# Performance work log

Hardware: AMD Instinct MI355X
Metric: run time of the kernel (lower is better)

## Reference

```python
import jax, jax.numpy as jnp
import numpy as np


def quat_to_rot(q):
    # q: [B, 4] = (x, y, z, w); same math as from_quaternion in the source.
    x, y, z, w = q[:, 0], q[:, 1], q[:, 2], q[:, 3]
    tx, ty, tz = 2.0 * x, 2.0 * y, 2.0 * z
    twx, twy, twz = tx * w, ty * w, tz * w
    txx, txy, txz = tx * x, ty * x, tz * x
    tyy, tyz, tzz = ty * y, tz * y, tz * z
    r = jnp.stack([1.0 - (tyy + tzz), txy - twz, txz + twy,
                   txy + twz, 1.0 - (txx + tzz), tyz - twx,
                   txz - twy, tyz + twx, 1.0 - (txx + tyy)], axis=-1)
    return r.reshape(-1, 3, 3)


def matrix_from_params(transfos):
    B, N = transfos.shape
    R = quat_to_rot(transfos[:, :4])
    if N == 10:
        S = jax.vmap(jnp.diag)(transfos[:, -3:])
    else:
        S = jnp.broadcast_to(jnp.eye(3, dtype=transfos.dtype), (B, 3, 3))
    SR = jnp.matmul(S, R)
    if N == 7:
        t = transfos[:, 4:7][..., None]
    else:
        t = jnp.zeros((B, 3, 1), transfos.dtype)
    return jnp.concatenate([SR, t], axis=2)  # [B, 3, 4]


def spatial_transformer_3d(img, transfos, min_ref_grid, max_ref_grid):
    B, H, W, D, C = img.shape  # ref_size_xyz = (W, H, D) per the source
    theta = matrix_from_params(transfos)  # [B, 3, 4]

    xs = jnp.linspace(min_ref_grid[0], max_ref_grid[0], W)
    ys = jnp.linspace(min_ref_grid[1], max_ref_grid[1], H)
    zs = jnp.linspace(min_ref_grid[2], max_ref_grid[2], D)
    mz, my, mx = jnp.meshgrid(zs, ys, xs, indexing='ij')  # (D, H, W), x fastest
    Nel = D * H * W
    grid = jnp.stack([mx.ravel(), my.ravel(), mz.ravel(),
                      jnp.ones(Nel, dtype=img.dtype)], axis=0)  # (4, Nel)
    pts = jnp.einsum('bij,jn->bin', theta, grid)  # (B, 3, Nel)

    Wf, Hf, Df = float(W), float(H), float(D)
    cx = (Wf - 1.0) / (max_ref_grid[0] - min_ref_grid[0])
    cy = (Hf - 1.0) / (max_ref_grid[1] - min_ref_grid[1])
    cz = (Df - 1.0) / (max_ref_grid[2] - min_ref_grid[2])
    ix = cx * pts[:, 0, :] - cx * min_ref_grid[0]
    iy = cy * pts[:, 1, :] - cy * min_ref_grid[1]
    iz = cz * pts[:, 2, :] - cz * min_ref_grid[2]

    # padding_mode in {'zeros','min'}: validity mask for out-of-grid points
    valid = ((ix >= 0.0) & (ix <= Wf - 1.0) &
             (iy >= 0.0) & (iy <= Hf - 1.0) &
             (iz >= 0.0) & (iz <= Df - 1.0)).astype(img.dtype)[..., None]  # (B, Nel, 1)

    ix0 = jnp.clip(jnp.floor(ix), 0.0, Wf - 1.0)
    iy0 = jnp.clip(jnp.floor(iy), 0.0, Hf - 1.0)
    iz0 = jnp.clip(jnp.floor(iz), 0.0, Df - 1.0)

    imf = img.reshape(B, H * W * D, C)
    acc = jnp.zeros((B, Nel, C), img.dtype)
    for ox in (0.0, 1.0):
        for oy in (0.0, 1.0):
            for oz in (0.0, 1.0):
                gx, gy, gz = ix0 + ox, iy0 + oy, iz0 + oz  # corner coords
                w = (jnp.clip(1.0 - jnp.abs(ix - gx), 0.0, 1.0) *
                     jnp.clip(1.0 - jnp.abs(iy - gy), 0.0, 1.0) *
                     jnp.clip(1.0 - jnp.abs(iz - gz), 0.0, 1.0))
                gxi = jnp.clip(gx, 0.0, Wf - 1.0).astype(jnp.int32)
                gyi = jnp.clip(gy, 0.0, Hf - 1.0).astype(jnp.int32)
                gzi = jnp.clip(gz, 0.0, Df - 1.0).astype(jnp.int32)
                lin = (gyi * W + gxi) * D + gzi  # row-major index into [H, W, D]
                v = jnp.take_along_axis(imf, lin[..., None], axis=1)  # (B, Nel, C)
                acc = acc + w[..., None] * v

    # padding_mode == 'min': fill out-of-grid voxels with the per-volume minimum
    fill = jnp.min(img, axis=(1, 2, 3, 4))[:, None, None]  # (B, 1, 1)
    out = valid * acc + (1.0 - valid) * fill
    # grid was flattened in (z, y, x) order with x fastest -> back to (H, W, D)
    out = out.reshape(B, D, H, W, C).transpose(0, 2, 3, 1, 4)
    return out


def setup_inputs() -> dict:
    key = jax.random.key(0)
    k1, k2 = jax.random.split(key)
    img = jax.random.normal(k1, (4, 160, 160, 160, 1), dtype=jnp.float32)
    transfos = jax.random.normal(k2, (4, 7), dtype=jnp.float32)
    return {"img": img, "transfos": transfos}


def reference(img, transfos):
    min_ref_grid = (-1.0, -1.0, -1.0)
    max_ref_grid = (1.0, 1.0, 1.0)
    return spatial_transformer_3d(img, transfos, min_ref_grid, max_ref_grid)
```

## Files before the change

### kernel.cpp

```cpp
#include <hip/hip_runtime.h>

#define HH 160
#define WW 160
#define DD 160
#define BB 4
#define NPB (HH * WW * DD / 4)
#define K1B 256
#define NTZ 10
#define NTX 20
#define NTY 20

typedef float vfloat4 __attribute__((ext_vector_type(4)));

__global__ __launch_bounds__(256) void min_cst_kernel(const float4* __restrict__ img4,
                                                      const float* __restrict__ transfos,
                                                      float* __restrict__ partial,
                                                      double* __restrict__ cst) {
    const int b = blockIdx.y;
    const size_t base = (size_t)b * NPB;
    const int t0 = blockIdx.x * 256 + threadIdx.x;
    const int S = K1B * 256;

    float m = 3.4e38f;
    #pragma unroll
    for (int r = 0; r < 4; r++) {
        const int i0 = t0 + 4 * r * S;
        float4 v0 = img4[base + i0];
        float4 v1 = img4[base + i0 + S];
        float4 v2 = img4[base + i0 + 2 * S];
        float4 v3 = make_float4(3.4e38f, 3.4e38f, 3.4e38f, 3.4e38f);
        if (i0 + 3 * S < NPB) v3 = img4[base + i0 + 3 * S];
        m = fminf(m, fminf(fminf(v0.x, v0.y), fminf(v0.z, v0.w)));
        m = fminf(m, fminf(fminf(v1.x, v1.y), fminf(v1.z, v1.w)));
        m = fminf(m, fminf(fminf(v2.x, v2.y), fminf(v2.z, v2.w)));
        m = fminf(m, fminf(fminf(v3.x, v3.y), fminf(v3.z, v3.w)));
    }

    #pragma unroll
    for (int o = 32; o >= 1; o >>= 1) m = fminf(m, __shfl_down(m, o));
    __shared__ float s[4];
    if ((threadIdx.x & 63) == 0) s[threadIdx.x >> 6] = m;
    __syncthreads();
    if (threadIdx.x == 0)
        partial[b * K1B + blockIdx.x] = fminf(fminf(s[0], s[1]), fminf(s[2], s[3]));

    if (blockIdx.x == 0 && blockIdx.y == 0 && threadIdx.x < BB) {
        const int bb = threadIdx.x;
        const float* q = transfos + bb * 7;
        double x = q[0], y = q[1], z = q[2], w = q[3];
        double tx = 2.0 * x, ty = 2.0 * y, tz = 2.0 * z;
        double twx = tx * w, twy = ty * w, twz = tz * w;
        double txx = tx * x, txy = ty * x, txz = tz * x;
        double tyy = ty * y, tyz = tz * y, tzz = tz * z;
        double R[3][3] = {
            {1.0 - (tyy + tzz), txy - twz,         txz + twy},
            {txy + twz,         1.0 - (txx + tzz), tyz - twx},
            {txz - twy,         tyz + twx,         1.0 - (txx + tyy)}
        };
        double t[3] = {(double)q[4], (double)q[5], (double)q[6]};
        for (int r = 0; r < 3; r++) {
            cst[bb * 12 + r * 4 + 0] = R[r][0];
            cst[bb * 12 + r * 4 + 1] = R[r][1];
            cst[bb * 12 + r * 4 + 2] = R[r][2];
            cst[bb * 12 + r * 4 + 3] = 79.5 * (t[r] - R[r][0] - R[r][1] - R[r][2] + 1.0);
        }
    }
}

__global__ __launch_bounds__(256) void fin_min_kernel(const float* __restrict__ partial,
                                                      float* __restrict__ fill) {
    const int wid = threadIdx.x >> 6, lane = threadIdx.x & 63;
    const float* p = partial + wid * K1B;
    float m = fminf(fminf(p[lane], p[lane + 64]), fminf(p[lane + 128], p[lane + 192]));
    #pragma unroll
    for (int o = 32; o >= 1; o >>= 1) m = fminf(m, __shfl_down(m, o));
    if (lane == 0) fill[wid] = m;
}

__device__ __forceinline__ bool tile_may_be_valid(const double* c, int xt, int yt, int zt) {
    const double X0 = (double)(xt * 8), X1 = X0 + 7.0;
    const double Y0 = (double)(yt * 8), Y1 = Y0 + 7.0;
    const double Z0 = (double)(zt * 16), Z1 = Z0 + 15.0;
    double lo, hi, t;

    lo = c[3]; hi = c[3];
    t = c[0]; if (t >= 0.0) { lo += t * X0; hi += t * X1; } else { lo += t * X1; hi += t * X0; }
    t = c[1]; if (t >= 0.0) { lo += t * Y0; hi += t * Y1; } else { lo += t * Y1; hi += t * Y0; }
    t = c[2]; if (t >= 0.0) { lo += t * Z0; hi += t * Z1; } else { lo += t * Z1; hi += t * Z0; }
    if (hi < -1e-3 || lo > 159.001) return false;

    lo = c[7]; hi = c[7];
    t = c[4]; if (t >= 0.0) { lo += t * X0; hi += t * X1; } else { lo += t * X1; hi += t * X0; }
    t = c[5]; if (t >= 0.0) { lo += t * Y0; hi += t * Y1; } else { lo += t * Y1; hi += t * Y0; }
    t = c[6]; if (t >= 0.0) { lo += t * Z0; hi += t * Z1; } else { lo += t * Z1; hi += t * Z0; }
    if (hi < -1e-3 || lo > 159.001) return false;

    lo = c[11]; hi = c[11];
    t = c[8]; if (t >= 0.0) { lo += t * X0; hi += t * X1; } else { lo += t * X1; hi += t * X0; }
    t = c[9]; if (t >= 0.0) { lo += t * Y0; hi += t * Y1; } else { lo += t * Y1; hi += t * Y0; }
    t = c[10]; if (t >= 0.0) { lo += t * Z0; hi += t * Z1; } else { lo += t * Z1; hi += t * Z0; }
    if (hi < -1e-3 || lo > 159.001) return false;
    return true;
}

__device__ __forceinline__ void gather_tile(const float* __restrict__ img,
                                            const double* __restrict__ c,
                                            float fillv, int b, int xt, int yt, int zt,
                                            int tid, float* __restrict__ out)
{
    const int tz = tid & 3;
    const int tx = (tid >> 2) & 7;
    const int ty = tid >> 5;
    const int x = xt * 8 + tx;
    const int y = yt * 8 + ty;
    const int zq = zt * 16 + tz * 4;

    const double c2 = c[2], c6 = c[6], c10 = c[10];
    const double dx = (double)x, dy = (double)y, dz = (double)zq;
    double ixd = fma(c[0], dx, fma(c[1], dy, fma(c2, dz, c[3])));
    double iyd = fma(c[4], dx, fma(c[5], dy, fma(c6, dz, c[7])));
    double izd = fma(c[8], dx, fma(c[9], dy, fma(c10, dz, c[11])));

    bool anyv = false;
    {
        double ax = ixd, ay = iyd, az = izd;
        #pragma unroll
        for (int k = 0; k < 4; k++) {
            anyv = anyv || ((ax >= 0.0) && (ax <= 159.0) && (ay >= 0.0) &&
                            (ay <= 159.0) && (az >= 0.0) && (az <= 159.0));
            ax += c2; ay += c6; az += c10;
        }
    }

    const float* base = img + (size_t)b * (HH * WW * DD);
    vfloat4 r;

    if (__any(anyv)) {
        #pragma unroll
        for (int k = 0; k < 4; k++) {
            const bool valid = (ixd >= 0.0) && (ixd <= 159.0) && (iyd >= 0.0) &&
                               (iyd <= 159.0) && (izd >= 0.0) && (izd <= 159.0);
            double flx = floor(ixd), fly = floor(iyd), flz = floor(izd);
            int x0 = (int)flx, y0 = (int)fly, z0 = (int)flz;
            x0 = min(max(x0, 0), 159);
            y0 = min(max(y0, 0), 159);
            z0 = min(max(z0, 0), 159);
            float fx = (float)(ixd - flx), fy = (float)(iyd - fly), fz = (float)(izd - flz);
            int x1 = min(x0 + 1, 159), y1 = min(y0 + 1, 159);
            const int zb = min(z0, 158);
            const bool ztop = (z0 == 159);
            const float* p00 = base + (y0 * WW + x0) * DD + zb;
            const float* p10 = base + (y1 * WW + x0) * DD + zb;
            const float* p01 = base + (y0 * WW + x1) * DD + zb;
            const float* p11 = base + (y1 * WW + x1) * DD + zb;
            float2 q00, q10, q01, q11;
            __builtin_memcpy(&q00, p00, 8);
            __builtin_memcpy(&q10, p10, 8);
            __builtin_memcpy(&q01, p01, 8);
            __builtin_memcpy(&q11, p11, 8);
            float v000 = ztop ? q00.y : q00.x, v001 = q00.y;
            float v010 = ztop ? q10.y : q10.x, v011 = q10.y;
            float v100 = ztop ? q01.y : q01.x, v101 = q01.y;
            float v110 = ztop ? q11.y : q11.x, v111 = q11.y;
            float wx0 = 1.0f - fx, wx1 = fx;
            float wy0 = 1.0f - fy, wy1 = fy;
            float wz0 = 1.0f - fz, wz1 = fz;
            float acc;
            acc  = ((wx0 * wy0) * wz0) * v000;
            acc += ((wx0 * wy0) * wz1) * v001;
            acc += ((wx0 * wy1) * wz0) * v010;
            acc += ((wx0 * wy1) * wz1) * v011;
            acc += ((wx1 * wy0) * wz0) * v100;
            acc += ((wx1 * wy0) * wz1) * v101;
            acc += ((wx1 * wy1) * wz0) * v110;
            acc += ((wx1 * wy1) * wz1) * v111;
            r[k] = valid ? acc : fillv;
            ixd += c2; iyd += c6; izd += c10;
        }
    } else {
        r[0] = fillv; r[1] = fillv; r[2] = fillv; r[3] = fillv;
    }

    __builtin_nontemporal_store(r, (vfloat4*)(out + (size_t)((b * HH + y) * WW + x) * DD + zq));
}

__global__ __launch_bounds__(256) void st3d_kernel(const float* __restrict__ img,
                                                   const double* __restrict__ cst,
                                                   const float* __restrict__ fill,
                                                   float* __restrict__ out) {
    const int bzc = blockIdx.z;
    const int b = bzc / NTY;
    const int yt = bzc - b * NTY;
    const int xt = blockIdx.y;
    const int zt = blockIdx.x;
    const double* c = cst + b * 12;
    const float fillv = fill[b];

    if (tile_may_be_valid(c, xt, yt, zt)) {
        gather_tile(img, c, fillv, b, xt, yt, zt, threadIdx.x, out);
    } else {
        vfloat4 v; v[0] = fillv; v[1] = fillv; v[2] = fillv; v[3] = fillv;
        const int tz = threadIdx.x & 3;
        const int tx = (threadIdx.x >> 2) & 7;
        const int ty = threadIdx.x >> 5;
        const int x = xt * 8 + tx;
        const int y = yt * 8 + ty;
        const int zq = zt * 16 + tz * 4;
        __builtin_nontemporal_store(v, (vfloat4*)(out + (size_t)((b * HH + y) * WW + x) * DD + zq));
    }
}

extern "C" void kernel_launch(void* const* d_in, const int* in_sizes, int n_in,
                              void* d_out, int out_size, void* d_ws, size_t ws_size,
                              hipStream_t stream) {
    const float* img = (const float*)d_in[0];
    const float* transfos = (const float*)d_in[1];
    float* out = (float*)d_out;
    float* partial = (float*)d_ws;
    double* cst = (double*)((char*)d_ws + 4096);
    float* fill = (float*)((char*)d_ws + 8192);

    min_cst_kernel<<<dim3(K1B, BB), 256, 0, stream>>>((const float4*)img, transfos,
                                                      partial, cst);
    fin_min_kernel<<<dim3(1), 256, 0, stream>>>(partial, fill);
    st3d_kernel<<<dim3(NTZ, NTX, NTY * BB), 256, 0, stream>>>(img, cst, fill, out);
}
```

Before: 129.2 us.

## Fuse min reduction with gather and defer fill writes to a second pass

The min-reduction blocks and the trilinear gather tiles now run in one launch, since the gather no longer needs the fill value: it writes only in-bounds voxels. A later kernel writes the per-volume minimum into out-of-grid voxels, skipping tiles that are fully inside. The min is combined with an atomicMin on an order-preserving unsigned encoding, which replaces the separate finalize kernel, and the transform constants are computed per block. This removes a serialising dependency and one launch, at the cost of a memset, partial scalar stores on boundary vectors, and repeated bounds math in the second kernel.

```diff
diff --git a/kernel.cpp b/kernel.cpp
--- a/kernel.cpp
+++ b/kernel.cpp
@@ -6,108 +6,123 @@
 #define BB 4
 #define NPB (HH * WW * DD / 4)
 #define K1B 256
+#define MINB (K1B * BB)
 #define NTZ 10
 #define NTX 20
 #define NTY 20
+#define NTILES (BB * NTY * NTX * NTZ)
 
 typedef float vfloat4 __attribute__((ext_vector_type(4)));
 
-__global__ __launch_bounds__(256) void min_cst_kernel(const float4* __restrict__ img4,
-                                                      const float* __restrict__ transfos,
-                                                      float* __restrict__ partial,
-                                                      double* __restrict__ cst) {
-    const int b = blockIdx.y;
-    const size_t base = (size_t)b * NPB;
-    const int t0 = blockIdx.x * 256 + threadIdx.x;
-    const int S = K1B * 256;
-
-    float m = 3.4e38f;
-    #pragma unroll
-    for (int r = 0; r < 4; r++) {
-        const int i0 = t0 + 4 * r * S;
-        float4 v0 = img4[base + i0];
-        float4 v1 = img4[base + i0 + S];
-        float4 v2 = img4[base + i0 + 2 * S];
-        float4 v3 = make_float4(3.4e38f, 3.4e38f, 3.4e38f, 3.4e38f);
-        if (i0 + 3 * S < NPB) v3 = img4[base + i0 + 3 * S];
-        m = fminf(m, fminf(fminf(v0.x, v0.y), fminf(v0.z, v0.w)));
-        m = fminf(m, fminf(fminf(v1.x, v1.y), fminf(v1.z, v1.w)));
-        m = fminf(m, fminf(fminf(v2.x, v2.y), fminf(v2.z, v2.w)));
-        m = fminf(m, fminf(fminf(v3.x, v3.y), fminf(v3.z, v3.w)));
-    }
-
-    #pragma unroll
-    for (int o = 32; o >= 1; o >>= 1) m = fminf(m, __shfl_down(m, o));
-    __shared__ float s[4];
-    if ((threadIdx.x & 63) == 0) s[threadIdx.x >> 6] = m;
-    __syncthreads();
-    if (threadIdx.x == 0)
-        partial[b * K1B + blockIdx.x] = fminf(fminf(s[0], s[1]), fminf(s[2], s[3]));
-
-    if (blockIdx.x == 0 && blockIdx.y == 0 && threadIdx.x < BB) {
-        const int bb = threadIdx.x;
-        const float* q = transfos + bb * 7;
-        double x = q[0], y = q[1], z = q[2], w = q[3];
-        double tx = 2.0 * x, ty = 2.0 * y, tz = 2.0 * z;
-        double twx = tx * w, twy = ty * w, twz = tz * w;
-        double txx = tx * x, txy = ty * x, txz = tz * x;
-        double tyy = ty * y, tyz = tz * y, tzz = tz * z;
-        double R[3][3] = {
-            {1.0 - (tyy + tzz), txy - twz,         txz + twy},
-            {txy + twz,         1.0 - (txx + tzz), tyz - twx},
-            {txz - twy,         tyz + twx,         1.0 - (txx + tyy)}
-        };
-        double t[3] = {(double)q[4], (double)q[5], (double)q[6]};
-        for (int r = 0; r < 3; r++) {
-            cst[bb * 12 + r * 4 + 0] = R[r][0];
-            cst[bb * 12 + r * 4 + 1] = R[r][1];
-            cst[bb * 12 + r * 4 + 2] = R[r][2];
-            cst[bb * 12 + r * 4 + 3] = 79.5 * (t[r] - R[r][0] - R[r][1] - R[r][2] + 1.0);
-        }
-    }
-}
-
-__global__ __launch_bounds__(256) void fin_min_kernel(const float* __restrict__ partial,
-                                                      float* __restrict__ fill) {
-    const int wid = threadIdx.x >> 6, lane = threadIdx.x & 63;
-    const float* p = partial + wid * K1B;
-    float m = fminf(fminf(p[lane], p[lane + 64]), fminf(p[lane + 128], p[lane + 192]));
-    #pragma unroll
-    for (int o = 32; o >= 1; o >>= 1) m = fminf(m, __shfl_down(m, o));
-    if (lane == 0) fill[wid] = m;
-}
-
-__device__ __forceinline__ bool tile_may_be_valid(const double* c, int xt, int yt, int zt) {
+__device__ __forceinline__ unsigned enc_f32(float f) {
+    unsigned u = __float_as_uint(f);
+    return u ^ ((u & 0x80000000u) ? 0xFFFFFFFFu : 0x80000000u);
+}
+__device__ __forceinline__ float dec_f32(unsigned e) {
+    return __uint_as_float(e ^ ((e & 0x80000000u) ? 0x80000000u : 0xFFFFFFFFu));
+}
+
+__device__ __forceinline__ void compute_cst(const float* __restrict__ transfos,
+                                            int b, double* __restrict__ c) {
+    const float* q = transfos + b * 7;
+    double x = q[0], y = q[1], z = q[2], w = q[3];
+    double tx = 2.0 * x, ty = 2.0 * y, tz = 2.0 * z;
+    double twx = tx * w, twy = ty * w, twz = tz * w;
+    double txx = tx * x, txy = ty * x, txz = tz * x;
+    double tyy = ty * y, tyz = tz * y, tzz = tz * z;
+    double R[3][3] = {
+        {1.0 - (tyy + tzz), txy - twz,         txz + twy},
+        {txy + twz,         1.0 - (txx + tzz), tyz - twx},
+        {txz - twy,         tyz + twx,         1.0 - (txx + tyy)}
+    };
+    double t[3] = {(double)q[4], (double)q[5], (double)q[6]};
+    #pragma unroll
+    for (int r = 0; r < 3; r++) {
+        c[r * 4 + 0] = R[r][0];
+        c[r * 4 + 1] = R[r][1];
+        c[r * 4 + 2] = R[r][2];
+        c[r * 4 + 3] = 79.5 * (t[r] - R[r][0] - R[r][1] - R[r][2] + 1.0);
+    }
+}
+
+__device__ __forceinline__ void tile_bounds(const double* __restrict__ c,
+                                            int xt, int yt, int zt,
+                                            double* __restrict__ lo,
+                                            double* __restrict__ hi) {
     const double X0 = (double)(xt * 8), X1 = X0 + 7.0;
     const double Y0 = (double)(yt * 8), Y1 = Y0 + 7.0;
     const double Z0 = (double)(zt * 16), Z1 = Z0 + 15.0;
-    double lo, hi, t;
-
-    lo = c[3]; hi = c[3];
-    t = c[0]; if (t >= 0.0) { lo += t * X0; hi += t * X1; } else { lo += t * X1; hi += t * X0; }
-    t = c[1]; if (t >= 0.0) { lo += t * Y0; hi += t * Y1; } else { lo += t * Y1; hi += t * Y0; }
-    t = c[2]; if (t >= 0.0) { lo += t * Z0; hi += t * Z1; } else { lo += t * Z1; hi += t * Z0; }
-    if (hi < -1e-3 || lo > 159.001) return false;
-
-    lo = c[7]; hi = c[7];
-    t = c[4]; if (t >= 0.0) { lo += t * X0; hi += t * X1; } else { lo += t * X1; hi += t * X0; }
-    t = c[5]; if (t >= 0.0) { lo += t * Y0; hi += t * Y1; } else { lo += t * Y1; hi += t * Y0; }
-    t = c[6]; if (t >= 0.0) { lo += t * Z0; hi += t * Z1; } else { lo += t * Z1; hi += t * Z0; }
-    if (hi < -1e-3 || lo > 159.001) return false;
-
-    lo = c[11]; hi = c[11];
-    t = c[8]; if (t >= 0.0) { lo += t * X0; hi += t * X1; } else { lo += t * X1; hi += t * X0; }
-    t = c[9]; if (t >= 0.0) { lo += t * Y0; hi += t * Y1; } else { lo += t * Y1; hi += t * Y0; }
-    t = c[10]; if (t >= 0.0) { lo += t * Z0; hi += t * Z1; } else { lo += t * Z1; hi += t * Z0; }
-    if (hi < -1e-3 || lo > 159.001) return false;
-    return true;
-}
-
-__device__ __forceinline__ void gather_tile(const float* __restrict__ img,
-                                            const double* __restrict__ c,
-                                            float fillv, int b, int xt, int yt, int zt,
-                                            int tid, float* __restrict__ out)
-{
+    #pragma unroll
+    for (int a = 0; a < 3; a++) {
+        double l = c[a * 4 + 3], h = c[a * 4 + 3], t;
+        t = c[a * 4 + 0]; if (t >= 0.0) { l += t * X0; h += t * X1; } else { l += t * X1; h += t * X0; }
+        t = c[a * 4 + 1]; if (t >= 0.0) { l += t * Y0; h += t * Y1; } else { l += t * Y1; h += t * Y0; }
+        t = c[a * 4 + 2]; if (t >= 0.0) { l += t * Z0; h += t * Z1; } else { l += t * Z1; h += t * Z0; }
+        lo[a] = l; hi[a] = h;
+    }
+}
+
+__global__ __launch_bounds__(256) void min_gather_kernel(const float* __restrict__ img,
+                                                         const float* __restrict__ transfos,
+                                                         unsigned* __restrict__ fillEnc,
+                                                         float* __restrict__ out) {
+    const int tid = threadIdx.x;
+    const int bid = blockIdx.x;
+
+    __shared__ double sc[12];
+    __shared__ int smaybe;
+    __shared__ float sred[4];
+
+    if (bid < MINB) {
+        const float4* img4 = (const float4*)img;
+        const int b = bid >> 8;
+        const size_t base = (size_t)b * NPB;
+        const int t0 = (bid & 255) * 256 + tid;
+        const int S = K1B * 256;
+        float m = 3.4e38f;
+        #pragma unroll
+        for (int r = 0; r < 4; r++) {
+            const int i0 = t0 + 4 * r * S;
+            float4 v0 = img4[base + i0];
+            float4 v1 = img4[base + i0 + S];
+            float4 v2 = img4[base + i0 + 2 * S];
+            float4 v3 = make_float4(3.4e38f, 3.4e38f, 3.4e38f, 3.4e38f);
+            if (i0 + 3 * S < NPB) v3 = img4[base + i0 + 3 * S];
+            m = fminf(m, fminf(fminf(v0.x, v0.y), fminf(v0.z, v0.w)));
+            m = fminf(m, fminf(fminf(v1.x, v1.y), fminf(v1.z, v1.w)));
+            m = fminf(m, fminf(fminf(v2.x, v2.y), fminf(v2.z, v2.w)));
+            m = fminf(m, fminf(fminf(v3.x, v3.y), fminf(v3.z, v3.w)));
+        }
+        #pragma unroll
+        for (int o = 32; o >= 1; o >>= 1) m = fminf(m, __shfl_down(m, o));
+        if ((tid & 63) == 0) sred[tid >> 6] = m;
+        __syncthreads();
+        if (tid == 0)
+            atomicMin(&fillEnc[b], enc_f32(fminf(fminf(sred[0], sred[1]),
+                                                 fminf(sred[2], sred[3]))));
+        return;
+    }
+
+    int tt = bid - MINB;
+    const int zt = tt % NTZ; tt /= NTZ;
+    const int xt = tt % NTX; tt /= NTX;
+    const int yt = tt % NTY;
+    const int b = tt / NTY;
+
+    if (tid == 0) {
+        double c[12];
+        compute_cst(transfos, b, c);
+        double lo[3], hi[3];
+        tile_bounds(c, xt, yt, zt, lo, hi);
+        smaybe = (hi[0] >= -1e-3 && lo[0] <= 159.001 &&
+                  hi[1] >= -1e-3 && lo[1] <= 159.001 &&
+                  hi[2] >= -1e-3 && lo[2] <= 159.001);
+        #pragma unroll
+        for (int j = 0; j < 12; j++) sc[j] = c[j];
+    }
+    __syncthreads();
+    if (!smaybe) return;
+
     const int tz = tid & 3;
     const int tx = (tid >> 2) & 7;
     const int ty = tid >> 5;
@@ -115,11 +130,14 @@
     const int y = yt * 8 + ty;
     const int zq = zt * 16 + tz * 4;
 
-    const double c2 = c[2], c6 = c[6], c10 = c[10];
+    const double c0 = sc[0], c1 = sc[1], c2 = sc[2], c3 = sc[3];
+    const double c4 = sc[4], c5 = sc[5], c6 = sc[6], c7 = sc[7];
+    const double c8 = sc[8], c9 = sc[9], c10 = sc[10], c11 = sc[11];
+
     const double dx = (double)x, dy = (double)y, dz = (double)zq;
-    double ixd = fma(c[0], dx, fma(c[1], dy, fma(c2, dz, c[3])));
-    double iyd = fma(c[4], dx, fma(c[5], dy, fma(c6, dz, c[7])));
-    double izd = fma(c[8], dx, fma(c[9], dy, fma(c10, dz, c[11])));
+    double ixd = fma(c0, dx, fma(c1, dy, fma(c2, dz, c3)));
+    double iyd = fma(c4, dx, fma(c5, dy, fma(c6, dz, c7)));
+    double izd = fma(c8, dx, fma(c9, dy, fma(c10, dz, c11)));
 
     bool anyv = false;
     {
@@ -131,83 +149,136 @@
             ax += c2; ay += c6; az += c10;
         }
     }
+    if (!__any(anyv)) return;
 
     const float* base = img + (size_t)b * (HH * WW * DD);
     vfloat4 r;
-
-    if (__any(anyv)) {
-        #pragma unroll
-        for (int k = 0; k < 4; k++) {
-            const bool valid = (ixd >= 0.0) && (ixd <= 159.0) && (iyd >= 0.0) &&
-                               (iyd <= 159.0) && (izd >= 0.0) && (izd <= 159.0);
-            double flx = floor(ixd), fly = floor(iyd), flz = floor(izd);
-            int x0 = (int)flx, y0 = (int)fly, z0 = (int)flz;
-            x0 = min(max(x0, 0), 159);
-            y0 = min(max(y0, 0), 159);
-            z0 = min(max(z0, 0), 159);
-            float fx = (float)(ixd - flx), fy = (float)(iyd - fly), fz = (float)(izd - flz);
-            int x1 = min(x0 + 1, 159), y1 = min(y0 + 1, 159);
-            const int zb = min(z0, 158);
-            const bool ztop = (z0 == 159);
-            const float* p00 = base + (y0 * WW + x0) * DD + zb;
-            const float* p10 = base + (y1 * WW + x0) * DD + zb;
-            const float* p01 = base + (y0 * WW + x1) * DD + zb;
-            const float* p11 = base + (y1 * WW + x1) * DD + zb;
-            float2 q00, q10, q01, q11;
-            __builtin_memcpy(&q00, p00, 8);
-            __builtin_memcpy(&q10, p10, 8);
-            __builtin_memcpy(&q01, p01, 8);
-            __builtin_memcpy(&q11, p11, 8);
-            float v000 = ztop ? q00.y : q00.x, v001 = q00.y;
-            float v010 = ztop ? q10.y : q10.x, v011 = q10.y;
-            float v100 = ztop ? q01.y : q01.x, v101 = q01.y;
-            float v110 = ztop ? q11.y : q11.x, v111 = q11.y;
-            float wx0 = 1.0f - fx, wx1 = fx;
-            float wy0 = 1.0f - fy, wy1 = fy;
-            float wz0 = 1.0f - fz, wz1 = fz;
-            float acc;
-            acc  = ((wx0 * wy0) * wz0) * v000;
-            acc += ((wx0 * wy0) * wz1) * v001;
-            acc += ((wx0 * wy1) * wz0) * v010;
-            acc += ((wx0 * wy1) * wz1) * v011;
-            acc += ((wx1 * wy0) * wz0) * v100;
-            acc += ((wx1 * wy0) * wz1) * v101;
-            acc += ((wx1 * wy1) * wz0) * v110;
-            acc += ((wx1 * wy1) * wz1) * v111;
-            r[k] = valid ? acc : fillv;
-            ixd += c2; iyd += c6; izd += c10;
-        }
+    unsigned mask = 0;
+    #pragma unroll
+    for (int k = 0; k < 4; k++) {
+        const bool valid = (ixd >= 0.0) && (ixd <= 159.0) && (iyd >= 0.0) &&
+                           (iyd <= 159.0) && (izd >= 0.0) && (izd <= 159.0);
+        if (valid) mask |= (1u << k);
+        double flx = floor(ixd), fly = floor(iyd), flz = floor(izd);
+        int x0 = (int)flx, y0 = (int)fly, z0 = (int)flz;
+        x0 = min(max(x0, 0), 159);
+        y0 = min(max(y0, 0), 159);
+        z0 = min(max(z0, 0), 159);
+        float fx = (float)(ixd - flx), fy = (float)(iyd - fly), fz = (float)(izd - flz);
+        int x1 = min(x0 + 1, 159), y1 = min(y0 + 1, 159);
+        const int zb = min(z0, 158);
+        const bool ztop = (z0 == 159);
+        const float* p00 = base + (y0 * WW + x0) * DD + zb;
+        const float* p10 = base + (y1 * WW + x0) * DD + zb;
+        const float* p01 = base + (y0 * WW + x1) * DD + zb;
+        const float* p11 = base + (y1 * WW + x1) * DD + zb;
+        float2 q00, q10, q01, q11;
+        __builtin_memcpy(&q00, p00, 8);
+        __builtin_memcpy(&q10, p10, 8);
+        __builtin_memcpy(&q01, p01, 8);
+        __builtin_memcpy(&q11, p11, 8);
+        float v000 = ztop ? q00.y : q00.x, v001 = q00.y;
+        float v010 = ztop ? q10.y : q10.x, v011 = q10.y;
+        float v100 = ztop ? q01.y : q01.x, v101 = q01.y;
+        float v110 = ztop ? q11.y : q11.x, v111 = q11.y;
+        float wx0 = 1.0f - fx, wx1 = fx;
+        float wy0 = 1.0f - fy, wy1 = fy;
+        float wz0 = 1.0f - fz, wz1 = fz;
+        float acc;
+        acc  = ((wx0 * wy0) * wz0) * v000;
+        acc += ((wx0 * wy0) * wz1) * v001;
+        acc += ((wx0 * wy1) * wz0) * v010;
+        acc += ((wx0 * wy1) * wz1) * v011;
+        acc += ((wx1 * wy0) * wz0) * v100;
+        acc += ((wx1 * wy0) * wz1) * v101;
+        acc += ((wx1 * wy1) * wz0) * v110;
+        acc += ((wx1 * wy1) * wz1) * v111;
+        r[k] = acc;
+        ixd += c2; iyd += c6; izd += c10;
+    }
+
+    float* op = out + (size_t)((b * HH + y) * WW + x) * DD + zq;
+    if (mask == 15u) {
+        __builtin_nontemporal_store(r, (vfloat4*)op);
     } else {
-        r[0] = fillv; r[1] = fillv; r[2] = fillv; r[3] = fillv;
-    }
-
-    __builtin_nontemporal_store(r, (vfloat4*)(out + (size_t)((b * HH + y) * WW + x) * DD + zq));
-}
-
-__global__ __launch_bounds__(256) void st3d_kernel(const float* __restrict__ img,
-                                                   const double* __restrict__ cst,
-                                                   const float* __restrict__ fill,
-                                                   float* __restrict__ out) {
+        if (mask & 1u) __builtin_nontemporal_store(r[0], op);
+        if (mask & 2u) __builtin_nontemporal_store(r[1], op + 1);
+        if (mask & 4u) __builtin_nontemporal_store(r[2], op + 2);
+        if (mask & 8u) __builtin_nontemporal_store(r[3], op + 3);
+    }
+}
+
+__global__ __launch_bounds__(256) void fill_inv_kernel(const float* __restrict__ transfos,
+                                                       const unsigned* __restrict__ fillEnc,
+                                                       float* __restrict__ out) {
     const int bzc = blockIdx.z;
     const int b = bzc / NTY;
     const int yt = bzc - b * NTY;
     const int xt = blockIdx.y;
     const int zt = blockIdx.x;
-    const double* c = cst + b * 12;
-    const float fillv = fill[b];
-
-    if (tile_may_be_valid(c, xt, yt, zt)) {
-        gather_tile(img, c, fillv, b, xt, yt, zt, threadIdx.x, out);
-    } else {
+    const int tid = threadIdx.x;
+
+    __shared__ double sc[12];
+    __shared__ int scls;
+    if (tid == 0) {
+        double c[12];
+        compute_cst(transfos, b, c);
+        double lo[3], hi[3];
+        tile_bounds(c, xt, yt, zt, lo, hi);
+        const bool maybe = (hi[0] >= -1e-3 && lo[0] <= 159.001 &&
+                            hi[1] >= -1e-3 && lo[1] <= 159.001 &&
+                            hi[2] >= -1e-3 && lo[2] <= 159.001);
+        const bool fully = (lo[0] >= 1e-3 && hi[0] <= 158.999 &&
+                            lo[1] >= 1e-3 && hi[1] <= 158.999 &&
+                            lo[2] >= 1e-3 && hi[2] <= 158.999);
+        scls = maybe ? (fully ? 2 : 1) : 0;
+        #pragma unroll
+        for (int j = 0; j < 12; j++) sc[j] = c[j];
+    }
+    __syncthreads();
+    const int cls = scls;
+    if (cls == 2) return;
+
+    const int tz = tid & 3;
+    const int tx = (tid >> 2) & 7;
+    const int ty = tid >> 5;
+    const int x = xt * 8 + tx;
+    const int y = yt * 8 + ty;
+    const int zq = zt * 16 + tz * 4;
+    float* op = out + (size_t)((b * HH + y) * WW + x) * DD + zq;
+    const float fillv = dec_f32(fillEnc[b]);
+
+    if (cls == 0) {
         vfloat4 v; v[0] = fillv; v[1] = fillv; v[2] = fillv; v[3] = fillv;
-        const int tz = threadIdx.x & 3;
-        const int tx = (threadIdx.x >> 2) & 7;
-        const int ty = threadIdx.x >> 5;
-        const int x = xt * 8 + tx;
-        const int y = yt * 8 + ty;
-        const int zq = zt * 16 + tz * 4;
-        __builtin_nontemporal_store(v, (vfloat4*)(out + (size_t)((b * HH + y) * WW + x) * DD + zq));
-    }
+        __builtin_nontemporal_store(v, (vfloat4*)op);
+        return;
+    }
+
+    const double c0 = sc[0], c1 = sc[1], c2 = sc[2], c3 = sc[3];
+    const double c4 = sc[4], c5 = sc[5], c6 = sc[6], c7 = sc[7];
+    const double c8 = sc[8], c9 = sc[9], c10 = sc[10], c11 = sc[11];
+    const double dx = (double)x, dy = (double)y, dz = (double)zq;
+    double ixd = fma(c0, dx, fma(c1, dy, fma(c2, dz, c3)));
+    double iyd = fma(c4, dx, fma(c5, dy, fma(c6, dz, c7)));
+    double izd = fma(c8, dx, fma(c9, dy, fma(c10, dz, c11)));
+    unsigned mask = 0;
+    #pragma unroll
+    for (int k = 0; k < 4; k++) {
+        const bool valid = (ixd >= 0.0) && (ixd <= 159.0) && (iyd >= 0.0) &&
+                           (iyd <= 159.0) && (izd >= 0.0) && (izd <= 159.0);
+        if (valid) mask |= (1u << k);
+        ixd += c2; iyd += c6; izd += c10;
+    }
+    if (mask == 15u) return;
+    if (mask == 0u) {
+        vfloat4 v; v[0] = fillv; v[1] = fillv; v[2] = fillv; v[3] = fillv;
+        __builtin_nontemporal_store(v, (vfloat4*)op);
+        return;
+    }
+    if (!(mask & 1u)) __builtin_nontemporal_store(fillv, op);
+    if (!(mask & 2u)) __builtin_nontemporal_store(fillv, op + 1);
+    if (!(mask & 4u)) __builtin_nontemporal_store(fillv, op + 2);
+    if (!(mask & 8u)) __builtin_nontemporal_store(fillv, op + 3);
 }
 
 extern "C" void kernel_launch(void* const* d_in, const int* in_sizes, int n_in,
@@ -216,12 +287,11 @@
     const float* img = (const float*)d_in[0];
     const float* transfos = (const float*)d_in[1];
     float* out = (float*)d_out;
-    float* partial = (float*)d_ws;
-    double* cst = (double*)((char*)d_ws + 4096);
-    float* fill = (float*)((char*)d_ws + 8192);
-
-    min_cst_kernel<<<dim3(K1B, BB), 256, 0, stream>>>((const float4*)img, transfos,
-                                                      partial, cst);
-    fin_min_kernel<<<dim3(1), 256, 0, stream>>>(partial, fill);
-    st3d_kernel<<<dim3(NTZ, NTX, NTY * BB), 256, 0, stream>>>(img, cst, fill, out);
-}
+    unsigned* fillEnc = (unsigned*)d_ws;
+
+    hipMemsetAsync(d_ws, 0xFF, 16, stream);
+    min_gather_kernel<<<dim3(MINB + NTILES), 256, 0, stream>>>(img, transfos,
+                                                               fillEnc, out);
+    fill_inv_kernel<<<dim3(NTZ, NTX, NTY * BB), 256, 0, stream>>>(transfos,
+                                                                  fillEnc, out);
+}
```

After: 134.9 us. 4.4% more time.

## Replace final min kernel with atomicMin and batch gather loads before interpolation

Applied to the files above, without the earlier changes.

Removes the separate final-reduction kernel. Each block now does an atomicMin on an order-preserving unsigned encoding of its float minimum, after a memset that initialises the slots to 0xFF. The gather loop is also split into a load phase and a compute phase separated by a sched_barrier, so all 16 loads per thread are issued before any arithmetic, for more memory-level parallelism. The cost is an extra memset launch, atomic contention across 256 blocks per batch, and higher register pressure.

```diff
diff --git a/kernel.cpp b/kernel.cpp
--- a/kernel.cpp
+++ b/kernel.cpp
@@ -9,12 +9,21 @@
 #define NTZ 10
 #define NTX 20
 #define NTY 20
+#define NTILES (BB * NTY * NTX * NTZ)
 
 typedef float vfloat4 __attribute__((ext_vector_type(4)));
+
+__device__ __forceinline__ unsigned enc_f32(float f) {
+    unsigned u = __float_as_uint(f);
+    return u ^ ((u & 0x80000000u) ? 0xFFFFFFFFu : 0x80000000u);
+}
+__device__ __forceinline__ float dec_f32(unsigned e) {
+    return __uint_as_float(e ^ ((e & 0x80000000u) ? 0x80000000u : 0xFFFFFFFFu));
+}
 
 __global__ __launch_bounds__(256) void min_cst_kernel(const float4* __restrict__ img4,
                                                       const float* __restrict__ transfos,
-                                                      float* __restrict__ partial,
+                                                      unsigned* __restrict__ fillEnc,
                                                       double* __restrict__ cst) {
     const int b = blockIdx.y;
     const size_t base = (size_t)b * NPB;
@@ -42,7 +51,7 @@
     if ((threadIdx.x & 63) == 0) s[threadIdx.x >> 6] = m;
     __syncthreads();
     if (threadIdx.x == 0)
-        partial[b * K1B + blockIdx.x] = fminf(fminf(s[0], s[1]), fminf(s[2], s[3]));
+        atomicMin(&fillEnc[b], enc_f32(fminf(fminf(s[0], s[1]), fminf(s[2], s[3]))));
 
     if (blockIdx.x == 0 && blockIdx.y == 0 && threadIdx.x < BB) {
         const int bb = threadIdx.x;
@@ -67,16 +76,6 @@
     }
 }
 
-__global__ __launch_bounds__(256) void fin_min_kernel(const float* __restrict__ partial,
-                                                      float* __restrict__ fill) {
-    const int wid = threadIdx.x >> 6, lane = threadIdx.x & 63;
-    const float* p = partial + wid * K1B;
-    float m = fminf(fminf(p[lane], p[lane + 64]), fminf(p[lane + 128], p[lane + 192]));
-    #pragma unroll
-    for (int o = 32; o >= 1; o >>= 1) m = fminf(m, __shfl_down(m, o));
-    if (lane == 0) fill[wid] = m;
-}
-
 __device__ __forceinline__ bool tile_may_be_valid(const double* c, int xt, int yt, int zt) {
     const double X0 = (double)(xt * 8), X1 = X0 + 7.0;
     const double Y0 = (double)(yt * 8), Y1 = Y0 + 7.0;
@@ -136,35 +135,49 @@
     vfloat4 r;
 
     if (__any(anyv)) {
+        float2 q00[4], q10[4], q01[4], q11[4];
+        float fxk[4], fyk[4], fzk[4];
+        unsigned vmask = 0, ztmask = 0;
+
         #pragma unroll
         for (int k = 0; k < 4; k++) {
             const bool valid = (ixd >= 0.0) && (ixd <= 159.0) && (iyd >= 0.0) &&
                                (iyd <= 159.0) && (izd >= 0.0) && (izd <= 159.0);
+            if (valid) vmask |= (1u << k);
             double flx = floor(ixd), fly = floor(iyd), flz = floor(izd);
             int x0 = (int)flx, y0 = (int)fly, z0 = (int)flz;
             x0 = min(max(x0, 0), 159);
             y0 = min(max(y0, 0), 159);
             z0 = min(max(z0, 0), 159);
-            float fx = (float)(ixd - flx), fy = (float)(iyd - fly), fz = (float)(izd - flz);
+            fxk[k] = (float)(ixd - flx);
+            fyk[k] = (float)(iyd - fly);
+            fzk[k] = (float)(izd - flz);
             int x1 = min(x0 + 1, 159), y1 = min(y0 + 1, 159);
             const int zb = min(z0, 158);
-            const bool ztop = (z0 == 159);
+            if (z0 == 159) ztmask |= (1u << k);
             const float* p00 = base + (y0 * WW + x0) * DD + zb;
             const float* p10 = base + (y1 * WW + x0) * DD + zb;
             const float* p01 = base + (y0 * WW + x1) * DD + zb;
             const float* p11 = base + (y1 * WW + x1) * DD + zb;
-            float2 q00, q10, q01, q11;
-            __builtin_memcpy(&q00, p00, 8);
-            __builtin_memcpy(&q10, p10, 8);
-            __builtin_memcpy(&q01, p01, 8);
-            __builtin_memcpy(&q11, p11, 8);
-            float v000 = ztop ? q00.y : q00.x, v001 = q00.y;
-            float v010 = ztop ? q10.y : q10.x, v011 = q10.y;
-            float v100 = ztop ? q01.y : q01.x, v101 = q01.y;
-            float v110 = ztop ? q11.y : q11.x, v111 = q11.y;
-            float wx0 = 1.0f - fx, wx1 = fx;
-            float wy0 = 1.0f - fy, wy1 = fy;
-            float wz0 = 1.0f - fz, wz1 = fz;
+            __builtin_memcpy(&q00[k], p00, 8);
+            __builtin_memcpy(&q10[k], p10, 8);
+            __builtin_memcpy(&q01[k], p01, 8);
+            __builtin_memcpy(&q11[k], p11, 8);
+            ixd += c2; iyd += c6; izd += c10;
+        }
+
+        __builtin_amdgcn_sched_barrier(0);
+
+        #pragma unroll
+        for (int k = 0; k < 4; k++) {
+            const bool ztop = (ztmask >> k) & 1u;
+            float v000 = ztop ? q00[k].y : q00[k].x, v001 = q00[k].y;
+            float v010 = ztop ? q10[k].y : q10[k].x, v011 = q10[k].y;
+            float v100 = ztop ? q01[k].y : q01[k].x, v101 = q01[k].y;
+            float v110 = ztop ? q11[k].y : q11[k].x, v111 = q11[k].y;
+            float wx0 = 1.0f - fxk[k], wx1 = fxk[k];
+            float wy0 = 1.0f - fyk[k], wy1 = fyk[k];
+            float wz0 = 1.0f - fzk[k], wz1 = fzk[k];
             float acc;
             acc  = ((wx0 * wy0) * wz0) * v000;
             acc += ((wx0 * wy0) * wz1) * v001;
@@ -174,8 +187,7 @@
             acc += ((wx1 * wy0) * wz1) * v101;
             acc += ((wx1 * wy1) * wz0) * v110;
             acc += ((wx1 * wy1) * wz1) * v111;
-            r[k] = valid ? acc : fillv;
-            ixd += c2; iyd += c6; izd += c10;
+            r[k] = ((vmask >> k) & 1u) ? acc : fillv;
         }
     } else {
         r[0] = fillv; r[1] = fillv; r[2] = fillv; r[3] = fillv;
@@ -186,7 +198,7 @@
 
 __global__ __launch_bounds__(256) void st3d_kernel(const float* __restrict__ img,
                                                    const double* __restrict__ cst,
-                                                   const float* __restrict__ fill,
+                                                   const unsigned* __restrict__ fillEnc,
                                                    float* __restrict__ out) {
     const int bzc = blockIdx.z;
     const int b = bzc / NTY;
@@ -194,7 +206,7 @@
     const int xt = blockIdx.y;
     const int zt = blockIdx.x;
     const double* c = cst + b * 12;
-    const float fillv = fill[b];
+    const float fillv = dec_f32(fillEnc[b]);
 
     if (tile_may_be_valid(c, xt, yt, zt)) {
         gather_tile(img, c, fillv, b, xt, yt, zt, threadIdx.x, out);
@@ -216,12 +228,11 @@
     const float* img = (const float*)d_in[0];
     const float* transfos = (const float*)d_in[1];
     float* out = (float*)d_out;
-    float* partial = (float*)d_ws;
+    unsigned* fillEnc = (unsigned*)d_ws;
     double* cst = (double*)((char*)d_ws + 4096);
-    float* fill = (float*)((char*)d_ws + 8192);
-
+
+    hipMemsetAsync(d_ws, 0xFF, 16, stream);
     min_cst_kernel<<<dim3(K1B, BB), 256, 0, stream>>>((const float4*)img, transfos,
-                                                      partial, cst);
-    fin_min_kernel<<<dim3(1), 256, 0, stream>>>(partial, fill);
-    st3d_kernel<<<dim3(NTZ, NTX, NTY * BB), 256, 0, stream>>>(img, cst, fill, out);
-}
+                                                      fillEnc, cst);
+    st3d_kernel<<<dim3(NTZ, NTX, NTY * BB), 256, 0, stream>>>(img, cst, fillEnc, out);
+}
```

Result: slower. 135.6 us (+5.0%).
